# Performance work log

Hardware: AMD Instinct MI355X
Metric: run time of the kernel (lower is better)

Reference implementation:

```python
import jax, jax.numpy as jnp
import numpy as np

B, I, O, D, H = 64, 1152, 32, 8, 16
NUM_ITERS = 3


def squash(s, axis=-1, eps=1e-08):
    sq = jnp.sum(s * s, axis=axis, keepdims=True)
    return (sq / (1.0 + sq)) * s / jnp.sqrt(sq + eps)


def setup_inputs() -> dict:
    key = jax.random.key(0)
    k1, k2 = jax.random.split(key)
    u = jax.random.normal(k1, (B, I, D), dtype=jnp.float32)
    weight = jax.random.normal(k2, (I, O, D, H), dtype=jnp.float32) * 0.1
    return {"u": u, "weight": weight}


def reference(u, weight):
    # u_hat: [b, i, o, h]
    u_hat = jnp.einsum('bid,iodh->bioh', u, weight)
    logits = jnp.zeros(u_hat.shape[:3], dtype=u_hat.dtype)

    def body(logits, _):
        coupling = jax.nn.softmax(logits, axis=-1)        # [b,i,o]
        s = jnp.einsum('bio,bioh->boh', coupling, u_hat)  # [b,o,h]
        v = squash(s)                                     # [b,o,h]
        logits = logits + jnp.einsum('boh,bioh->bio', v, u_hat)
        return logits, v

    _, vs = jax.lax.scan(body, logits, None, length=NUM_ITERS)
    return vs[-1]
```

## Files before the change

### kernel.cpp

```cpp
#include <hip/hip_runtime.h>

#define BB 64
#define II 1152
#define OO 32
#define DD 8
#define HH 16
#define BOH (BB * OO * HH)
#define WTILE (OO * DD * HH)

#define IC   9
#define NIC  128
#define NBB  16
#define NBG  4
#define NJB  4

template<int CTRL>
__device__ __forceinline__ float dpp_add(float x)
{
    return x + __int_as_float(__builtin_amdgcn_update_dpp(
            0, __float_as_int(x), CTRL, 0xF, 0xF, false));
}

__device__ __forceinline__ float row_sum16(float x)
{
    x = dpp_add<0x121>(x);
    x = dpp_add<0x122>(x);
    x = dpp_add<0x124>(x);
    x = dpp_add<0x128>(x);
    return x;
}

__device__ __forceinline__ float add_xor32(float x)
{
#if __has_builtin(__builtin_amdgcn_permlane32_swap)
    auto r = __builtin_amdgcn_permlane32_swap(
        __float_as_uint(x), __float_as_uint(x), false, false);
    return __uint_as_float(r[0]) + __uint_as_float(r[1]);
#else
    return x + __shfl_xor(x, 32, 64);
#endif
}

__device__ __forceinline__ float add_xor16(float x)
{
#if __has_builtin(__builtin_amdgcn_permlane16_swap)
    auto r = __builtin_amdgcn_permlane16_swap(
        __float_as_uint(x), __float_as_uint(x), false, false);
    return __uint_as_float(r[0]) + __uint_as_float(r[1]);
#else
    return x + __int_as_float(__builtin_amdgcn_ds_swizzle(__float_as_int(x), 0x401F));
#endif
}

__device__ __forceinline__ int wswz(int f) { return f ^ (((f >> 7) & 31) << 2); }

__device__ __forceinline__ void stage_w_tile(const float* __restrict__ wg,
                                             float* __restrict__ wn, int tid)
{
    #pragma unroll
    for (int j = 0; j < 4; j++) {
        const int P = (tid + j * 256) * 4;
        const int g = wswz(P);
        __builtin_amdgcn_global_load_lds(
            (const __attribute__((address_space(1))) void*)(wg + g),
            (__attribute__((address_space(3))) void*)(wn + P),
            16, 0, 0);
    }
}

template<int PASS, bool ATOMIC>
__global__ __launch_bounds__(256)
void pass_kernel(const float* __restrict__ u, const float* __restrict__ w,
                 const float* __restrict__ pv0, const float* __restrict__ pv1,
                 float* __restrict__ out)
{
    __shared__ __align__(16) float Wsh[2][WTILE];

    const int tid   = threadIdx.x;
    const int o     = tid & 31;
    const int hh    = (tid >> 5) & 1;
    const int bq    = tid >> 6;
    const int bbase = blockIdx.y * NBB;
    const int i0    = blockIdx.x * IC;
    const int hofs  = hh * 8;
    const int swm   = o << 2;
    const int orow  = o * (DD * HH);

    stage_w_tile(w + (size_t)i0 * WTILE, Wsh[0], tid);

    float vsum[NJB][8];
    if (PASS >= 1) {
        #pragma unroll
        for (int jb = 0; jb < NJB; jb++) {
            const int b = bbase + bq * NJB + jb;
            const float* p = pv0 + ((b * OO + o) * HH + hofs);
            float4 a = *(const float4*)p;
            float4 c = *(const float4*)(p + 4);
            vsum[jb][0] = a.x; vsum[jb][1] = a.y; vsum[jb][2] = a.z; vsum[jb][3] = a.w;
            vsum[jb][4] = c.x; vsum[jb][5] = c.y; vsum[jb][6] = c.z; vsum[jb][7] = c.w;
            if (PASS == 2) {
                const float* q = pv1 + ((b * OO + o) * HH + hofs);
                float4 a2 = *(const float4*)q;
                float4 c2 = *(const float4*)(q + 4);
                vsum[jb][0] += a2.x; vsum[jb][1] += a2.y; vsum[jb][2] += a2.z; vsum[jb][3] += a2.w;
                vsum[jb][4] += c2.x; vsum[jb][5] += c2.y; vsum[jb][6] += c2.z; vsum[jb][7] += c2.w;
            }
        }
    }

    float sacc[NJB][8];
    #pragma unroll
    for (int jb = 0; jb < NJB; jb++)
        #pragma unroll
        for (int h2 = 0; h2 < 8; h2++) sacc[jb][h2] = 0.f;

    __syncthreads();

    for (int ii = 0; ii < IC; ii++) {
        const float* wcur = Wsh[ii & 1];

        if (ii + 1 < IC)
            stage_w_tile(w + (size_t)(i0 + ii + 1) * WTILE, Wsh[(ii + 1) & 1], tid);

        float us[NJB][8];
        #pragma unroll
        for (int jb = 0; jb < NJB; jb++) {
            const float* ub = u + ((size_t)(bbase + bq * NJB + jb) * II + (i0 + ii)) * DD;
            float4 a = *(const float4*)ub;
            float4 c = *(const float4*)(ub + 4);
            us[jb][0] = a.x; us[jb][1] = a.y; us[jb][2] = a.z; us[jb][3] = a.w;
            us[jb][4] = c.x; us[jb][5] = c.y; us[jb][6] = c.z; us[jb][7] = c.w;
        }

        float uh[NJB][8];
        #pragma unroll
        for (int jb = 0; jb < NJB; jb++)
            #pragma unroll
            for (int h2 = 0; h2 < 8; h2++) uh[jb][h2] = 0.f;
        #pragma unroll
        for (int d = 0; d < DD; d++) {
            const int ba = (d * HH + hofs    ) ^ swm;
            const int bb = (d * HH + hofs + 4) ^ swm;
            float4 wa = *(const float4*)&wcur[orow + ba];
            float4 wb = *(const float4*)&wcur[orow + bb];
            const float wv[8] = {wa.x, wa.y, wa.z, wa.w, wb.x, wb.y, wb.z, wb.w};
            #pragma unroll
            for (int jb = 0; jb < NJB; jb++)
                #pragma unroll
                for (int h2 = 0; h2 < 8; h2++)
                    uh[jb][h2] = fmaf(us[jb][d], wv[h2], uh[jb][h2]);
        }

        float cc[NJB];
        if (PASS == 0) {
            #pragma unroll
            for (int jb = 0; jb < NJB; jb++) cc[jb] = 1.0f / 32.0f;
        } else {
            #pragma unroll
            for (int jb = 0; jb < NJB; jb++) {
                float lg = 0.f;
                #pragma unroll
                for (int h2 = 0; h2 < 8; h2++)
                    lg = fmaf(vsum[jb][h2], uh[jb][h2], lg);
                lg = add_xor32(lg);
                const float e = __expf(lg);
                const float se = add_xor16(row_sum16(e));
                cc[jb] = __fdividef(e, se);
            }
        }

        #pragma unroll
        for (int jb = 0; jb < NJB; jb++)
            #pragma unroll
            for (int h2 = 0; h2 < 8; h2++)
                sacc[jb][h2] = fmaf(cc[jb], uh[jb][h2], sacc[jb][h2]);

        __syncthreads();
    }

    #pragma unroll
    for (int jb = 0; jb < NJB; jb++) {
        const int b = bbase + bq * NJB + jb;
        if (ATOMIC) {
            float* p = out + ((b * OO + o) * HH + hofs);
            #pragma unroll
            for (int h2 = 0; h2 < 8; h2++) atomicAdd(p + h2, sacc[jb][h2]);
        } else {
            float* p = out + ((size_t)blockIdx.x * BB + b) * (OO * HH) + o * HH + hofs;
            *(float4*)p       = make_float4(sacc[jb][0], sacc[jb][1], sacc[jb][2], sacc[jb][3]);
            *(float4*)(p + 4) = make_float4(sacc[jb][4], sacc[jb][5], sacc[jb][6], sacc[jb][7]);
        }
    }
}

__global__ __launch_bounds__(256)
void reduce_squash_wide_kernel(const float* __restrict__ part, float* __restrict__ v)
{
    const int t4l = threadIdx.x & 31;
    const int icp = threadIdx.x >> 5;
    const int t4  = blockIdx.x * 32 + t4l;

    const float4* p = (const float4*)part + t4;
    float4 acc = make_float4(0.f, 0.f, 0.f, 0.f);
    #pragma unroll
    for (int k = 0; k < NIC / 8; k++) {
        float4 x = p[(size_t)(icp * (NIC / 8) + k) * (BOH / 4)];
        acc.x += x.x; acc.y += x.y; acc.z += x.z; acc.w += x.w;
    }

    __shared__ float4 red[8][32];
    red[icp][t4l] = acc;
    __syncthreads();

    if (threadIdx.x < 32) {
        float4 a = red[0][t4l];
        #pragma unroll
        for (int j = 1; j < 8; j++) {
            float4 x = red[j][t4l];
            a.x += x.x; a.y += x.y; a.z += x.z; a.w += x.w;
        }
        float sq = a.x * a.x + a.y * a.y + a.z * a.z + a.w * a.w;
        sq = dpp_add<0xB1>(sq);
        sq = dpp_add<0x4E>(sq);
        const float scale = (sq / (1.f + sq)) * rsqrtf(sq + 1e-8f);
        a.x *= scale; a.y *= scale; a.z *= scale; a.w *= scale;
        ((float4*)v)[t4] = a;
    }
}

__global__ __launch_bounds__(256)
void squash_kernel(const float* __restrict__ s, float* __restrict__ v)
{
    const int t = blockIdx.x * blockDim.x + threadIdx.x;
    if (t >= BB * OO) return;
    const float4* sp = (const float4*)(s + t * HH);
    float4 a = sp[0], b = sp[1], c = sp[2], d = sp[3];
    float sq = a.x*a.x + a.y*a.y + a.z*a.z + a.w*a.w
             + b.x*b.x + b.y*b.y + b.z*b.z + b.w*b.w
             + c.x*c.x + c.y*c.y + c.z*c.z + c.w*c.w
             + d.x*d.x + d.y*d.y + d.z*d.z + d.w*d.w;
    const float scale = (sq / (1.f + sq)) * rsqrtf(sq + 1e-8f);
    a.x *= scale; a.y *= scale; a.z *= scale; a.w *= scale;
    b.x *= scale; b.y *= scale; b.z *= scale; b.w *= scale;
    c.x *= scale; c.y *= scale; c.z *= scale; c.w *= scale;
    d.x *= scale; d.y *= scale; d.z *= scale; d.w *= scale;
    float4* vp = (float4*)(v + t * HH);
    vp[0] = a; vp[1] = b; vp[2] = c; vp[3] = d;
}

extern "C" void kernel_launch(void* const* d_in, const int* in_sizes, int n_in,
                              void* d_out, int out_size, void* d_ws, size_t ws_size,
                              hipStream_t stream)
{
    (void)in_sizes; (void)n_in; (void)out_size;
    const float* u = (const float*)d_in[0];
    const float* w = (const float*)d_in[1];
    float* out = (float*)d_out;

    const size_t need = ((size_t)NIC * BOH + 2 * BOH) * sizeof(float);
    const dim3 grid(NIC, NBG), blk(256);

    if (ws_size >= need) {
        float* part = (float*)d_ws;
        float* v0   = part + (size_t)NIC * BOH;
        float* v1   = v0 + BOH;
        const int rblocks = BOH / 4 / 32;

        pass_kernel<0, false><<<grid, blk, 0, stream>>>(u, w, nullptr, nullptr, part);
        reduce_squash_wide_kernel<<<rblocks, 256, 0, stream>>>(part, v0);
        pass_kernel<1, false><<<grid, blk, 0, stream>>>(u, w, v0, nullptr, part);
        reduce_squash_wide_kernel<<<rblocks, 256, 0, stream>>>(part, v1);
        pass_kernel<2, false><<<grid, blk, 0, stream>>>(u, w, v0, v1, part);
        reduce_squash_wide_kernel<<<rblocks, 256, 0, stream>>>(part, out);
    } else {
        float* s0 = (float*)d_ws;
        float* s1 = s0 + BOH;
        float* v0 = s1 + BOH;
        float* v1 = v0 + BOH;
        hipMemsetAsync(d_ws, 0, 2 * BOH * sizeof(float), stream);
        hipMemsetAsync(d_out, 0, BOH * sizeof(float), stream);
        const int sq_blocks = (BB * OO + 255) / 256;

        pass_kernel<0, true><<<grid, blk, 0, stream>>>(u, w, nullptr, nullptr, s0);
        squash_kernel<<<sq_blocks, 256, 0, stream>>>(s0, v0);
        pass_kernel<1, true><<<grid, blk, 0, stream>>>(u, w, v0, nullptr, s1);
        squash_kernel<<<sq_blocks, 256, 0, stream>>>(s1, v1);
        pass_kernel<2, true><<<grid, blk, 0, stream>>>(u, w, v0, v1, out);
        squash_kernel<<<sq_blocks, 256, 0, stream>>>(out, out);
    }
}
```

Before: 137.1 us.

## Fuse three routing passes and reductions into one cooperative persistent kernel

Replaces the six-launch sequence (three pass kernels and three reduce/squash kernels) with a single cooperative kernel. It uses a hierarchical atomic grid barrier between the partial-sum write, the reduction/squash step and the next pass. The grid is halved to 64x4 blocks, each handling 18 input capsules, so all blocks can be co-resident and the partial reduction shrinks to 64 slices. This removes launch gaps and inter-kernel drains, at the cost of fewer blocks (less parallelism and latency hiding), spin-wait barrier overhead, and reliance on cooperative launch support with a fallback path.

```diff
diff --git a/kernel.cpp b/kernel.cpp
--- a/kernel.cpp
+++ b/kernel.cpp
@@ -8,11 +8,17 @@
 #define BOH (BB * OO * HH)
 #define WTILE (OO * DD * HH)
 
-#define IC   9
-#define NIC  128
 #define NBB  16
 #define NBG  4
 #define NJB  4
+
+#define IC_F   9
+#define NIC_F  128
+
+#define IC_C   18
+#define NIC_C  64
+#define NBLK_C (NIC_C * NBG)
+#define NGRP_C (NBLK_C / 64)
 
 template<int CTRL>
 __device__ __forceinline__ float dpp_add(float x)
@@ -68,6 +74,195 @@
     }
 }
 
+__device__ __forceinline__ void gbar(unsigned* __restrict__ bar, int phase, int bi)
+{
+    __syncthreads();
+    if (threadIdx.x == 0) {
+        __threadfence_system();
+        unsigned* grp    = bar + (bi >> 6);
+        unsigned* master = bar + 8;
+        unsigned* gen    = bar + 9;
+        const unsigned a = __hip_atomic_fetch_add(grp, 1u, __ATOMIC_ACQ_REL,
+                                                  __HIP_MEMORY_SCOPE_AGENT) + 1;
+        if (a == (unsigned)((phase + 1) * 64)) {
+            const unsigned m = __hip_atomic_fetch_add(master, 1u, __ATOMIC_ACQ_REL,
+                                                      __HIP_MEMORY_SCOPE_AGENT) + 1;
+            if (m == (unsigned)((phase + 1) * NGRP_C)) {
+                __hip_atomic_store(gen, (unsigned)(phase + 1), __ATOMIC_RELEASE,
+                                   __HIP_MEMORY_SCOPE_AGENT);
+            }
+        }
+        while (__hip_atomic_load(gen, __ATOMIC_ACQUIRE,
+                                 __HIP_MEMORY_SCOPE_AGENT) < (unsigned)(phase + 1)) {
+            __builtin_amdgcn_s_sleep(2);
+        }
+        __threadfence_system();
+    }
+    __syncthreads();
+}
+
+__global__ __launch_bounds__(256)
+void routing_kernel(const float* __restrict__ u, const float* __restrict__ w,
+                    float* __restrict__ part, float* __restrict__ v0,
+                    float* __restrict__ v1, float* __restrict__ out,
+                    unsigned* __restrict__ bar)
+{
+    __shared__ __align__(16) float Wsh[2][WTILE];
+    __shared__ float4 red[8][32];
+
+    const int tid   = threadIdx.x;
+    const int o     = tid & 31;
+    const int hh    = (tid >> 5) & 1;
+    const int bq    = tid >> 6;
+    const int bx    = blockIdx.x;
+    const int by    = blockIdx.y;
+    const int bi    = by * NIC_C + bx;
+    const int bbase = by * NBB;
+    const int i0    = bx * IC_C;
+    const int hofs  = hh * 8;
+    const int swm   = o << 2;
+    const int orow  = o * (DD * HH);
+
+    int phase = 0;
+
+    for (int p = 0; p < 3; ++p) {
+        float vsum[NJB][8];
+        if (p >= 1) {
+            #pragma unroll
+            for (int jb = 0; jb < NJB; jb++) {
+                const int b = bbase + bq * NJB + jb;
+                const float* pp = v0 + ((b * OO + o) * HH + hofs);
+                float4 a = *(const float4*)pp;
+                float4 c = *(const float4*)(pp + 4);
+                vsum[jb][0] = a.x; vsum[jb][1] = a.y; vsum[jb][2] = a.z; vsum[jb][3] = a.w;
+                vsum[jb][4] = c.x; vsum[jb][5] = c.y; vsum[jb][6] = c.z; vsum[jb][7] = c.w;
+                if (p == 2) {
+                    const float* q = v1 + ((b * OO + o) * HH + hofs);
+                    float4 a2 = *(const float4*)q;
+                    float4 c2 = *(const float4*)(q + 4);
+                    vsum[jb][0] += a2.x; vsum[jb][1] += a2.y; vsum[jb][2] += a2.z; vsum[jb][3] += a2.w;
+                    vsum[jb][4] += c2.x; vsum[jb][5] += c2.y; vsum[jb][6] += c2.z; vsum[jb][7] += c2.w;
+                }
+            }
+        }
+
+        stage_w_tile(w + (size_t)i0 * WTILE, Wsh[0], tid);
+
+        float sacc[NJB][8];
+        #pragma unroll
+        for (int jb = 0; jb < NJB; jb++)
+            #pragma unroll
+            for (int h2 = 0; h2 < 8; h2++) sacc[jb][h2] = 0.f;
+
+        __syncthreads();
+
+        for (int ii = 0; ii < IC_C; ii++) {
+            const float* wcur = Wsh[ii & 1];
+            if (ii + 1 < IC_C)
+                stage_w_tile(w + (size_t)(i0 + ii + 1) * WTILE, Wsh[(ii + 1) & 1], tid);
+
+            float us[NJB][8];
+            #pragma unroll
+            for (int jb = 0; jb < NJB; jb++) {
+                const float* ub = u + ((size_t)(bbase + bq * NJB + jb) * II + (i0 + ii)) * DD;
+                float4 a = *(const float4*)ub;
+                float4 c = *(const float4*)(ub + 4);
+                us[jb][0] = a.x; us[jb][1] = a.y; us[jb][2] = a.z; us[jb][3] = a.w;
+                us[jb][4] = c.x; us[jb][5] = c.y; us[jb][6] = c.z; us[jb][7] = c.w;
+            }
+
+            float uh[NJB][8];
+            #pragma unroll
+            for (int jb = 0; jb < NJB; jb++)
+                #pragma unroll
+                for (int h2 = 0; h2 < 8; h2++) uh[jb][h2] = 0.f;
+            #pragma unroll
+            for (int d = 0; d < DD; d++) {
+                const int ba  = (d * HH + hofs    ) ^ swm;
+                const int bb2 = (d * HH + hofs + 4) ^ swm;
+                float4 wa = *(const float4*)&wcur[orow + ba];
+                float4 wb = *(const float4*)&wcur[orow + bb2];
+                const float wv[8] = {wa.x, wa.y, wa.z, wa.w, wb.x, wb.y, wb.z, wb.w};
+                #pragma unroll
+                for (int jb = 0; jb < NJB; jb++)
+                    #pragma unroll
+                    for (int h2 = 0; h2 < 8; h2++)
+                        uh[jb][h2] = fmaf(us[jb][d], wv[h2], uh[jb][h2]);
+            }
+
+            float cc[NJB];
+            if (p == 0) {
+                #pragma unroll
+                for (int jb = 0; jb < NJB; jb++) cc[jb] = 1.0f / 32.0f;
+            } else {
+                #pragma unroll
+                for (int jb = 0; jb < NJB; jb++) {
+                    float lg = 0.f;
+                    #pragma unroll
+                    for (int h2 = 0; h2 < 8; h2++)
+                        lg = fmaf(vsum[jb][h2], uh[jb][h2], lg);
+                    lg = add_xor32(lg);
+                    const float e = __expf(lg);
+                    const float se = add_xor16(row_sum16(e));
+                    cc[jb] = __fdividef(e, se);
+                }
+            }
+
+            #pragma unroll
+            for (int jb = 0; jb < NJB; jb++)
+                #pragma unroll
+                for (int h2 = 0; h2 < 8; h2++)
+                    sacc[jb][h2] = fmaf(cc[jb], uh[jb][h2], sacc[jb][h2]);
+
+            __syncthreads();
+        }
+
+        #pragma unroll
+        for (int jb = 0; jb < NJB; jb++) {
+            const int b = bbase + bq * NJB + jb;
+            float* pp = part + ((size_t)bx * BB + b) * (OO * HH) + o * HH + hofs;
+            *(float4*)pp       = make_float4(sacc[jb][0], sacc[jb][1], sacc[jb][2], sacc[jb][3]);
+            *(float4*)(pp + 4) = make_float4(sacc[jb][4], sacc[jb][5], sacc[jb][6], sacc[jb][7]);
+        }
+
+        gbar(bar, phase++, bi);
+
+        {
+            float* vt = (p == 0) ? v0 : (p == 1) ? v1 : out;
+            const int t4l = tid & 31;
+            const int icp = tid >> 5;
+            const int t4  = bi * 32 + t4l;
+
+            const float4* pr = (const float4*)part + t4;
+            float4 acc = make_float4(0.f, 0.f, 0.f, 0.f);
+            #pragma unroll
+            for (int k = 0; k < 8; k++) {
+                float4 x = pr[(size_t)(icp * 8 + k) * (BOH / 4)];
+                acc.x += x.x; acc.y += x.y; acc.z += x.z; acc.w += x.w;
+            }
+            red[icp][t4l] = acc;
+            __syncthreads();
+
+            if (tid < 32) {
+                float4 a = red[0][t4l];
+                #pragma unroll
+                for (int j = 1; j < 8; j++) {
+                    float4 x = red[j][t4l];
+                    a.x += x.x; a.y += x.y; a.z += x.z; a.w += x.w;
+                }
+                float sq = a.x * a.x + a.y * a.y + a.z * a.z + a.w * a.w;
+                sq = dpp_add<0xB1>(sq);
+                sq = dpp_add<0x4E>(sq);
+                const float scale = (sq / (1.f + sq)) * rsqrtf(sq + 1e-8f);
+                a.x *= scale; a.y *= scale; a.z *= scale; a.w *= scale;
+                ((float4*)vt)[t4] = a;
+            }
+        }
+
+        if (p < 2) gbar(bar, phase++, bi);
+    }
+}
+
 template<int PASS, bool ATOMIC>
 __global__ __launch_bounds__(256)
 void pass_kernel(const float* __restrict__ u, const float* __restrict__ w,
@@ -81,7 +276,7 @@
     const int hh    = (tid >> 5) & 1;
     const int bq    = tid >> 6;
     const int bbase = blockIdx.y * NBB;
-    const int i0    = blockIdx.x * IC;
+    const int i0    = blockIdx.x * IC_F;
     const int hofs  = hh * 8;
     const int swm   = o << 2;
     const int orow  = o * (DD * HH);
@@ -116,10 +311,9 @@
 
     __syncthreads();
 
-    for (int ii = 0; ii < IC; ii++) {
+    for (int ii = 0; ii < IC_F; ii++) {
         const float* wcur = Wsh[ii & 1];
-
-        if (ii + 1 < IC)
+        if (ii + 1 < IC_F)
             stage_w_tile(w + (size_t)(i0 + ii + 1) * WTILE, Wsh[(ii + 1) & 1], tid);
 
         float us[NJB][8];
@@ -139,10 +333,10 @@
             for (int h2 = 0; h2 < 8; h2++) uh[jb][h2] = 0.f;
         #pragma unroll
         for (int d = 0; d < DD; d++) {
-            const int ba = (d * HH + hofs    ) ^ swm;
-            const int bb = (d * HH + hofs + 4) ^ swm;
+            const int ba  = (d * HH + hofs    ) ^ swm;
+            const int bb2 = (d * HH + hofs + 4) ^ swm;
             float4 wa = *(const float4*)&wcur[orow + ba];
-            float4 wb = *(const float4*)&wcur[orow + bb];
+            float4 wb = *(const float4*)&wcur[orow + bb2];
             const float wv[8] = {wa.x, wa.y, wa.z, wa.w, wb.x, wb.y, wb.z, wb.w};
             #pragma unroll
             for (int jb = 0; jb < NJB; jb++)
@@ -203,8 +397,8 @@
     const float4* p = (const float4*)part + t4;
     float4 acc = make_float4(0.f, 0.f, 0.f, 0.f);
     #pragma unroll
-    for (int k = 0; k < NIC / 8; k++) {
-        float4 x = p[(size_t)(icp * (NIC / 8) + k) * (BOH / 4)];
+    for (int k = 0; k < NIC_F / 8; k++) {
+        float4 x = p[(size_t)(icp * (NIC_F / 8) + k) * (BOH / 4)];
         acc.x += x.x; acc.y += x.y; acc.z += x.z; acc.w += x.w;
     }
 
@@ -257,21 +451,43 @@
     const float* w = (const float*)d_in[1];
     float* out = (float*)d_out;
 
-    const size_t need = ((size_t)NIC * BOH + 2 * BOH) * sizeof(float);
-    const dim3 grid(NIC, NBG), blk(256);
+    const size_t partN = (size_t)NIC_F * BOH;
+    const size_t need  = (partN + 2 * BOH + 64) * sizeof(float);
 
     if (ws_size >= need) {
-        float* part = (float*)d_ws;
-        float* v0   = part + (size_t)NIC * BOH;
-        float* v1   = v0 + BOH;
-        const int rblocks = BOH / 4 / 32;
-
-        pass_kernel<0, false><<<grid, blk, 0, stream>>>(u, w, nullptr, nullptr, part);
-        reduce_squash_wide_kernel<<<rblocks, 256, 0, stream>>>(part, v0);
-        pass_kernel<1, false><<<grid, blk, 0, stream>>>(u, w, v0, nullptr, part);
-        reduce_squash_wide_kernel<<<rblocks, 256, 0, stream>>>(part, v1);
-        pass_kernel<2, false><<<grid, blk, 0, stream>>>(u, w, v0, v1, part);
-        reduce_squash_wide_kernel<<<rblocks, 256, 0, stream>>>(part, out);
+        float* part   = (float*)d_ws;
+        float* v0     = part + partN;
+        float* v1     = v0 + BOH;
+        unsigned* bar = (unsigned*)(v1 + BOH);
+
+        bool done = false;
+        int dev = 0, coop = 0;
+        if (hipGetDevice(&dev) == hipSuccess)
+            (void)hipDeviceGetAttribute(&coop, hipDeviceAttributeCooperativeLaunch, dev);
+        if (coop) {
+            hipMemsetAsync(bar, 0, 16 * sizeof(unsigned), stream);
+            void* args[] = {
+                (void*)&u, (void*)&w, (void*)&part, (void*)&v0,
+                (void*)&v1, (void*)&out, (void*)&bar
+            };
+            hipError_t e = hipLaunchCooperativeKernel(
+                reinterpret_cast<void*>(routing_kernel),
+                dim3(NIC_C, NBG), dim3(256), args, 0, stream);
+            if (e == hipSuccess) done = true;
+            else (void)hipGetLastError();
+        }
+
+        if (!done) {
+            const dim3 grid(NIC_F, NBG), blk(256);
+            const int rblocks = BOH / 4 / 32;
+
+            pass_kernel<0, false><<<grid, blk, 0, stream>>>(u, w, nullptr, nullptr, part);
+            reduce_squash_wide_kernel<<<rblocks, 256, 0, stream>>>(part, v0);
+            pass_kernel<1, false><<<grid, blk, 0, stream>>>(u, w, v0, nullptr, part);
+            reduce_squash_wide_kernel<<<rblocks, 256, 0, stream>>>(part, v1);
+            pass_kernel<2, false><<<grid, blk, 0, stream>>>(u, w, v0, v1, part);
+            reduce_squash_wide_kernel<<<rblocks, 256, 0, stream>>>(part, out);
+        }
     } else {
         float* s0 = (float*)d_ws;
         float* s1 = s0 + BOH;
@@ -279,6 +495,7 @@
         float* v1 = v0 + BOH;
         hipMemsetAsync(d_ws, 0, 2 * BOH * sizeof(float), stream);
         hipMemsetAsync(d_out, 0, BOH * sizeof(float), stream);
+        const dim3 grid(NIC_F, NBG), blk(256);
         const int sq_blocks = (BB * OO + 255) / 256;
 
         pass_kernel<0, true><<<grid, blk, 0, stream>>>(u, w, nullptr, nullptr, s0);
```

Measured after the change: 403.3 us. +194.1%, slower.
